# Performance work log

Hardware: AMD Instinct MI355X
Metric: run time of the kernel (lower is better)

Reference implementation:

```python
import jax, jax.numpy as jnp
import numpy as np
from jax import lax

N, H, W, C = 4, 256, 256, 128
COUT = 128
BS_IN, BS_OUT, BSTR = 18, 16, 16  # gather block, conv-out block, block stride
N_ACTIVE = 512


def setup_inputs() -> dict:
    key = jax.random.key(0)
    ks = jax.random.split(key, 8)
    x = jax.random.normal(ks[0], (N, H, W, C), dtype=jnp.float32)
    w = jax.random.normal(ks[1], (3, 3, C, COUT), dtype=jnp.float32) * 0.05  # HWIO
    b = jax.random.normal(ks[2], (COUT,), dtype=jnp.float32) * 0.05
    gamma = jax.random.uniform(ks[3], (COUT,), dtype=jnp.float32, minval=0.5, maxval=1.5)
    beta = jax.random.normal(ks[4], (COUT,), dtype=jnp.float32) * 0.1
    mean = jax.random.normal(ks[5], (COUT,), dtype=jnp.float32) * 0.1
    var = jax.random.uniform(ks[6], (COUT,), dtype=jnp.float32, minval=0.5, maxval=1.5)
    # unique active block ids over the N x (H/16) x (W/16) grid -> disjoint scatter targets
    n_blocks = N * (H // BSTR) * (W // BSTR)
    active = jax.random.permutation(ks[7], n_blocks)[:N_ACTIVE].astype(jnp.int32)
    return {"x": x, "w": w, "b": b, "gamma": gamma, "beta": beta,
            "mean": mean, "var": var, "active": active}


def reference(x, w, b, gamma, beta, mean, var, active):
    n_, h_, w_, c_ = x.shape
    nby, nbx = h_ // BSTR, w_ // BSTR
    bn = active // (nby * nbx)
    rem = active % (nby * nbx)
    by = rem // nbx
    bx = rem % nbx

    # --- sparse_gather: overlapping BS_IN x BS_IN input blocks (zero-pad edges) ---
    pad = BS_IN - BS_OUT
    xp = jnp.pad(x, ((0, 0), (0, pad), (0, pad), (0, 0)))
    Hp, Wp = h_ + pad, w_ + pad
    d_in = jnp.arange(BS_IN, dtype=jnp.int32)
    hs = by[:, None] * BSTR + d_in[None, :]            # [Nb, 18]
    ws = bx[:, None] * BSTR + d_in[None, :]            # [Nb, 18]
    gidx = bn[:, None, None] * (Hp * Wp) + hs[:, :, None] * Wp + ws[:, None, :]
    p = xp.reshape(-1, c_)[gidx]                       # [Nb, 18, 18, C]

    # --- dense conv + BN(eval, eps=1e-3) + ReLU on gathered blocks ---
    q = lax.conv_general_dilated(p, w, window_strides=(1, 1), padding='VALID',
                                 dimension_numbers=('NHWC', 'HWIO', 'NHWC'))
    q = q + b
    q = (q - mean) * (gamma * lax.rsqrt(var + 1e-3)) + beta
    q = jax.nn.relu(q)                                 # [Nb, 16, 16, COUT]

    # --- sparse_scatter: write disjoint BS_OUT blocks back into a copy of x ---
    d_out = jnp.arange(BS_OUT, dtype=jnp.int32)
    hso = by[:, None] * BSTR + d_out[None, :]
    wso = bx[:, None] * BSTR + d_out[None, :]
    sidx = bn[:, None, None] * (h_ * w_) + hso[:, :, None] * w_ + wso[:, None, :]
    y = x.reshape(-1, c_).at[sidx.reshape(-1)].set(q.reshape(-1, q.shape[-1]))
    return y.reshape(n_, h_, w_, c_)
```

## Files before the change

### kernel.cpp

```cpp
#include <hip/hip_runtime.h>
#include <hip/hip_bf16.h>

#define H_ 256
#define W_ 256
#define C_ 128
#define NBPOS 1024
#define NACT 512

typedef __bf16 bf16x8 __attribute__((ext_vector_type(8)));
typedef float f32x4 __attribute__((ext_vector_type(4)));

#define SCALE_OFF 294912
#define SHIFT_OFF 295424
#define INACT_OFF 295936

__global__ void prep_kernel(const float* __restrict__ w, const float* __restrict__ b,
                            const float* __restrict__ gamma, const float* __restrict__ beta,
                            const float* __restrict__ mean, const float* __restrict__ var,
                            const int* __restrict__ active,
                            __bf16* __restrict__ wprep, float* __restrict__ scale,
                            float* __restrict__ shift, int* __restrict__ inact) {
  int blk = blockIdx.x, tid = threadIdx.x;
  if (blk < 576) {
    int o = blk * 256 + tid;
    int j = o & 7, cout = (o >> 3) & 127, k8 = (o >> 10) & 15, tap = o >> 14;
    wprep[o] = (__bf16)w[((size_t)tap * 128 + k8 * 8 + j) * 128 + cout];
    return;
  }
  __shared__ unsigned mask[32];
  __shared__ int cnt;
  if (tid < 32) mask[tid] = 0u;
  if (tid == 0) cnt = 0;
  __syncthreads();
  for (int i = tid; i < NACT; i += 256) {
    int a = active[i];
    atomicOr(&mask[a >> 5], 1u << (a & 31));
  }
  if (tid < 128) {
    float s = gamma[tid] * rsqrtf(var[tid] + 1e-3f);
    scale[tid] = s;
    shift[tid] = (b[tid] - mean[tid]) * s + beta[tid];
  }
  __syncthreads();
  for (int p = tid; p < NBPOS; p += 256) {
    if (!((mask[p >> 5] >> (p & 31)) & 1u)) {
      int q = atomicAdd(&cnt, 1);
      inact[q] = p;
    }
  }
}

__global__ __launch_bounds__(256, 4) void main_kernel(
    const float* __restrict__ x, const __bf16* __restrict__ wprep,
    const float* __restrict__ scale, const float* __restrict__ shift,
    const int* __restrict__ active, const int* __restrict__ inact,
    float* __restrict__ y) {
  __shared__ unsigned char ldsA[180 * 128];
  __shared__ unsigned char ldsB[2][8192];

  const int idx = blockIdx.x;
  const int tid = threadIdx.x;

  if (idx % 3 == 2) {
    const int cid = inact[idx / 3];
    const int cn = cid >> 8, cy = (cid >> 4) & 15, cx = cid & 15;
    const size_t base4 = ((((size_t)cn * H_ + cy * 16) * W_ + cx * 16) * C_) >> 2;
    const f32x4* __restrict__ xs = (const f32x4*)x;
    f32x4* __restrict__ ys = (f32x4*)y;
#pragma unroll 4
    for (int i = 0; i < 32; ++i) {
      int lin = (i << 8) + tid;
      int row = lin >> 9, rem = lin & 511;
      size_t idx4 = base4 + (size_t)row * (W_ * C_ / 4) + rem;
      f32x4 v = xs[idx4];
      __builtin_nontemporal_store(v, &ys[idx4]);
    }
    return;
  }

  const int j = (idx / 3) * 2 + (idx % 3);
  const int lane = tid & 63;
  const int wid = tid >> 6;
  const int aid = active[j >> 1];
  const int mh = j & 1;
  const int bn = aid >> 8, by = (aid >> 4) & 15, bx = aid & 15;
  const int h0 = by * 16, w0 = bx * 16;
  const int hm = h0 + mh * 8;
  const float* xb = x + (size_t)bn * (H_ * W_ * C_);

  f32x4 acc[2][8];
  f32x4 zero = {0.f, 0.f, 0.f, 0.f};
#pragma unroll
  for (int i = 0; i < 2; ++i)
#pragma unroll
    for (int jj = 0; jj < 8; ++jj) acc[i][jj] = zero;

  const uint4* wp4 = (const uint4*)wprep;
  uint4 t0, t1;
  auto load_t = [&](int u) {
    int ks = u % 18, h = u / 18;
    int tile = ((ks >> 1) << 2) + (h << 1) + (ks & 1);
    t0 = wp4[tile * 512 + tid];
    t1 = wp4[tile * 512 + 256 + tid];
  };
  auto stage = [&](int half) {
    for (int u = tid; u < 180 * 8; u += 256) {
      int s = u >> 3, c8 = u & 7;
      int pr = s / 18, col = s - pr * 18;
      int hs = hm + pr, wsp = w0 + col;
      float4 f0 = make_float4(0.f, 0.f, 0.f, 0.f), f1 = f0;
      if (hs < H_ && wsp < W_) {
        const float* p = xb + (size_t)(hs * W_ + wsp) * C_ + half * 64 + c8 * 8;
        f0 = *(const float4*)p;
        f1 = *(const float4*)(p + 4);
      }
      bf16x8 v;
      v[0] = (__bf16)f0.x; v[1] = (__bf16)f0.y; v[2] = (__bf16)f0.z; v[3] = (__bf16)f0.w;
      v[4] = (__bf16)f1.x; v[5] = (__bf16)f1.y; v[6] = (__bf16)f1.z; v[7] = (__bf16)f1.w;
      int lin = s * 128 + c8 * 16;
      *(bf16x8*)(&ldsA[lin ^ ((s & 7) << 4)]) = v;
    }
  };

  load_t(0);
  stage(0);
  ((uint4*)ldsB[0])[tid] = t0;
  ((uint4*)ldsB[0])[256 + tid] = t1;
  load_t(1);
  __syncthreads();

  const int koff = (lane >> 4) * 16;
  const int colb = (lane & 15) * 16;
  const int krow = (lane >> 4) * 2048;

  for (int u = 0; u < 36; ++u) {
    int cur = u & 1;
    if (u < 35) {
      ((uint4*)ldsB[cur ^ 1])[tid] = t0;
      ((uint4*)ldsB[cur ^ 1])[256 + tid] = t1;
      if (u < 34) load_t(u + 2);
    }
    int ks = u % 18;
    int tap = ks >> 1, kch = ks & 1;
    int dyv = tap / 3, dxv = tap - dyv * 3;

    bf16x8 a[2];
#pragma unroll
    for (int mi = 0; mi < 2; ++mi) {
      int srow = (wid * 2 + mi + dyv) * 18 + dxv + (lane & 15);
      int lin = srow * 128 + kch * 64 + koff;
      a[mi] = *(const bf16x8*)(&ldsA[lin ^ ((srow & 7) << 4)]);
    }
    bf16x8 bfr[8];
#pragma unroll
    for (int nb = 0; nb < 8; ++nb)
      bfr[nb] = *(const bf16x8*)(&ldsB[cur][krow + nb * 256 + colb]);
#pragma unroll
    for (int mi = 0; mi < 2; ++mi)
#pragma unroll
      for (int nb = 0; nb < 8; ++nb)
        acc[mi][nb] = __builtin_amdgcn_mfma_f32_16x16x32_bf16(a[mi], bfr[nb], acc[mi][nb], 0, 0, 0);

    __syncthreads();
    if (u == 17) {
      stage(1);
      __syncthreads();
    }
  }

  const int colc = lane & 15;
  float sc[8], sh[8];
#pragma unroll
  for (int nb = 0; nb < 8; ++nb) {
    sc[nb] = scale[nb * 16 + colc];
    sh[nb] = shift[nb * 16 + colc];
  }
  float* yb = y + (((size_t)bn * H_ + hm) * W_ + w0) * C_;
#pragma unroll
  for (int mi = 0; mi < 2; ++mi) {
    int oy = wid * 2 + mi;
#pragma unroll
    for (int r = 0; r < 4; ++r) {
      int ox = (lane >> 4) * 4 + r;
      float* yr = yb + ((size_t)oy * W_ + ox) * C_;
#pragma unroll
      for (int nb = 0; nb < 8; ++nb) {
        float v = acc[mi][nb][r] * sc[nb] + sh[nb];
        __builtin_nontemporal_store(fmaxf(v, 0.f), &yr[nb * 16 + colc]);
      }
    }
  }
}

extern "C" void kernel_launch(void* const* d_in, const int* in_sizes, int n_in,
                              void* d_out, int out_size, void* d_ws, size_t ws_size,
                              hipStream_t stream) {
  const float* x     = (const float*)d_in[0];
  const float* w     = (const float*)d_in[1];
  const float* b     = (const float*)d_in[2];
  const float* gamma = (const float*)d_in[3];
  const float* beta  = (const float*)d_in[4];
  const float* mean  = (const float*)d_in[5];
  const float* var   = (const float*)d_in[6];
  const int*   act   = (const int*)d_in[7];
  float* y = (float*)d_out;
  char* ws = (char*)d_ws;
  __bf16* wprep = (__bf16*)ws;
  float* scale = (float*)(ws + SCALE_OFF);
  float* shift = (float*)(ws + SHIFT_OFF);
  int* inact = (int*)(ws + INACT_OFF);

  prep_kernel<<<dim3(577), dim3(256), 0, stream>>>(w, b, gamma, beta, mean, var, act,
                                                   wprep, scale, shift, inact);
  main_kernel<<<dim3(1536), dim3(256), 0, stream>>>(x, wprep, scale, shift, act, inact, y);
}
```

Measured before the change: 75.26 us.

## Use 2x2 wave tiling for MFMA and split copy blocks into halves

The conv GEMM wave layout changes from each wave owning 2 output rows by all 8 column tiles to a 2x2 arrangement where each wave owns 4 rows by 4 column tiles. This reduces LDS B-fragment reads per wave while A reads grow, balancing LDS traffic. The inactive-block copy work is split into two half-blocks, each using batched 8-wide loads before stores to raise memory-level parallelism. Grid grows to 2048 blocks, interleaving compute and copy blocks evenly.

After: 81.41 us. +8.2%, slower.

```diff
diff --git a/kernel.cpp b/kernel.cpp
--- a/kernel.cpp
+++ b/kernel.cpp
@@ -61,26 +61,37 @@
   const int idx = blockIdx.x;
   const int tid = threadIdx.x;
 
-  if (idx % 3 == 2) {
-    const int cid = inact[idx / 3];
+  if (idx & 1) {
+    const int k = idx >> 1;
+    const int cid = inact[k >> 1];
+    const int ch = k & 1;
     const int cn = cid >> 8, cy = (cid >> 4) & 15, cx = cid & 15;
-    const size_t base4 = ((((size_t)cn * H_ + cy * 16) * W_ + cx * 16) * C_) >> 2;
+    const size_t base4 = ((((size_t)cn * H_ + cy * 16 + ch * 8) * W_ + cx * 16) * C_) >> 2;
     const f32x4* __restrict__ xs = (const f32x4*)x;
     f32x4* __restrict__ ys = (f32x4*)y;
-#pragma unroll 4
-    for (int i = 0; i < 32; ++i) {
-      int lin = (i << 8) + tid;
-      int row = lin >> 9, rem = lin & 511;
-      size_t idx4 = base4 + (size_t)row * (W_ * C_ / 4) + rem;
-      f32x4 v = xs[idx4];
-      __builtin_nontemporal_store(v, &ys[idx4]);
+#pragma unroll
+    for (int b = 0; b < 2; ++b) {
+      f32x4 v[8];
+#pragma unroll
+      for (int q = 0; q < 8; ++q) {
+        int lin = (b * 8 + q) * 256 + tid;
+        size_t i4 = base4 + (size_t)(lin >> 9) * (W_ * C_ / 4) + (lin & 511);
+        v[q] = xs[i4];
+      }
+#pragma unroll
+      for (int q = 0; q < 8; ++q) {
+        int lin = (b * 8 + q) * 256 + tid;
+        size_t i4 = base4 + (size_t)(lin >> 9) * (W_ * C_ / 4) + (lin & 511);
+        __builtin_nontemporal_store(v[q], &ys[i4]);
+      }
     }
     return;
   }
 
-  const int j = (idx / 3) * 2 + (idx % 3);
+  const int j = idx >> 1;
   const int lane = tid & 63;
   const int wid = tid >> 6;
+  const int wr = wid >> 1, wc = wid & 1;
   const int aid = active[j >> 1];
   const int mh = j & 1;
   const int bn = aid >> 8, by = (aid >> 4) & 15, bx = aid & 15;
@@ -88,12 +99,12 @@
   const int hm = h0 + mh * 8;
   const float* xb = x + (size_t)bn * (H_ * W_ * C_);
 
-  f32x4 acc[2][8];
+  f32x4 acc[4][4];
   f32x4 zero = {0.f, 0.f, 0.f, 0.f};
 #pragma unroll
-  for (int i = 0; i < 2; ++i)
-#pragma unroll
-    for (int jj = 0; jj < 8; ++jj) acc[i][jj] = zero;
+  for (int i = 0; i < 4; ++i)
+#pragma unroll
+    for (int jj = 0; jj < 4; ++jj) acc[i][jj] = zero;
 
   const uint4* wp4 = (const uint4*)wprep;
   uint4 t0, t1;
@@ -144,21 +155,21 @@
     int tap = ks >> 1, kch = ks & 1;
     int dyv = tap / 3, dxv = tap - dyv * 3;
 
-    bf16x8 a[2];
-#pragma unroll
-    for (int mi = 0; mi < 2; ++mi) {
-      int srow = (wid * 2 + mi + dyv) * 18 + dxv + (lane & 15);
+    bf16x8 a[4];
+#pragma unroll
+    for (int mi = 0; mi < 4; ++mi) {
+      int srow = (wr * 4 + mi + dyv) * 18 + dxv + (lane & 15);
       int lin = srow * 128 + kch * 64 + koff;
       a[mi] = *(const bf16x8*)(&ldsA[lin ^ ((srow & 7) << 4)]);
     }
-    bf16x8 bfr[8];
-#pragma unroll
-    for (int nb = 0; nb < 8; ++nb)
-      bfr[nb] = *(const bf16x8*)(&ldsB[cur][krow + nb * 256 + colb]);
-#pragma unroll
-    for (int mi = 0; mi < 2; ++mi)
-#pragma unroll
-      for (int nb = 0; nb < 8; ++nb)
+    bf16x8 bfr[4];
+#pragma unroll
+    for (int nb = 0; nb < 4; ++nb)
+      bfr[nb] = *(const bf16x8*)(&ldsB[cur][krow + (wc * 4 + nb) * 256 + colb]);
+#pragma unroll
+    for (int mi = 0; mi < 4; ++mi)
+#pragma unroll
+      for (int nb = 0; nb < 4; ++nb)
         acc[mi][nb] = __builtin_amdgcn_mfma_f32_16x16x32_bf16(a[mi], bfr[nb], acc[mi][nb], 0, 0, 0);
 
     __syncthreads();
@@ -169,24 +180,24 @@
   }
 
   const int colc = lane & 15;
-  float sc[8], sh[8];
-#pragma unroll
-  for (int nb = 0; nb < 8; ++nb) {
-    sc[nb] = scale[nb * 16 + colc];
-    sh[nb] = shift[nb * 16 + colc];
+  float sc[4], sh[4];
+#pragma unroll
+  for (int nb = 0; nb < 4; ++nb) {
+    sc[nb] = scale[(wc * 4 + nb) * 16 + colc];
+    sh[nb] = shift[(wc * 4 + nb) * 16 + colc];
   }
   float* yb = y + (((size_t)bn * H_ + hm) * W_ + w0) * C_;
 #pragma unroll
-  for (int mi = 0; mi < 2; ++mi) {
-    int oy = wid * 2 + mi;
+  for (int mi = 0; mi < 4; ++mi) {
+    int oy = wr * 4 + mi;
 #pragma unroll
     for (int r = 0; r < 4; ++r) {
       int ox = (lane >> 4) * 4 + r;
       float* yr = yb + ((size_t)oy * W_ + ox) * C_;
 #pragma unroll
-      for (int nb = 0; nb < 8; ++nb) {
+      for (int nb = 0; nb < 4; ++nb) {
         float v = acc[mi][nb][r] * sc[nb] + sh[nb];
-        __builtin_nontemporal_store(fmaxf(v, 0.f), &yr[nb * 16 + colc]);
+        __builtin_nontemporal_store(fmaxf(v, 0.f), &yr[(wc * 4 + nb) * 16 + colc]);
       }
     }
   }
@@ -212,5 +223,5 @@
 
   prep_kernel<<<dim3(577), dim3(256), 0, stream>>>(w, b, gamma, beta, mean, var, act,
                                                    wprep, scale, shift, inact);
-  main_kernel<<<dim3(1536), dim3(256), 0, stream>>>(x, wprep, scale, shift, act, inact, y);
+  main_kernel<<<dim3(2048), dim3(256), 0, stream>>>(x, wprep, scale, shift, act, inact, y);
 }
```
